# Kernel tuning notes

Measured on AMD Instinct MI355X. Metric: run time of the kernel, lower is better.

Reference implementation:

```python
import jax, jax.numpy as jnp
import numpy as np

K = 3
STRIDE = 1
PAD = 1
C_IN = 128
C_OUT = 128
B, H, W = 4, 128, 128


def conv2d(x, w, b, stride, pad):
    # x: (B,C,H,W), w: (O,I,kh,kw)
    out = jax.lax.conv_general_dilated(
        x, w, window_strides=(stride, stride),
        padding=[(pad, pad), (pad, pad)],
        dimension_numbers=("NCHW", "OIHW", "NCHW"))
    return out + b[None, :, None, None]


def bilinear_sample(img, ix, iy):
    # img: (C,H,W); ix, iy: (N,) float pixel coords.
    # Bilinear, padding_mode='zeros', align_corners=False semantics.
    C, Hc, Wc = img.shape
    x0 = jnp.floor(ix).astype(jnp.int32)
    y0 = jnp.floor(iy).astype(jnp.int32)
    x1 = x0 + 1
    y1 = y0 + 1
    wx1 = ix - x0.astype(img.dtype)
    wy1 = iy - y0.astype(img.dtype)
    wx0 = 1.0 - wx1
    wy0 = 1.0 - wy1

    def gather(yi, xi):
        valid = ((yi >= 0) & (yi < Hc) & (xi >= 0) & (xi < Wc)).astype(img.dtype)
        v = img[:, jnp.clip(yi, 0, Hc - 1), jnp.clip(xi, 0, Wc - 1)]  # (C,N)
        return v * valid[None, :]

    return (gather(y0, x0) * (wy0 * wx0)[None]
            + gather(y0, x1) * (wy0 * wx1)[None]
            + gather(y1, x0) * (wy1 * wx0)[None]
            + gather(y1, x1) * (wy1 * wx1)[None])


def setup_inputs() -> dict:
    key = jax.random.key(0)
    k1, k2, k3 = jax.random.split(key, 3)
    x = jax.random.normal(k1, (B, C_IN, H, W), dtype=jnp.float32)
    # offset conv: small random so grid_sample does real irregular gathers
    w_off = jax.random.normal(k2, (2 * K * K, C_IN, K, K), dtype=jnp.float32) * 0.01
    b_off = jnp.zeros((2 * K * K,), dtype=jnp.float32)
    # main conv: kaiming normal, fan_out = C_OUT*K*K
    std = float(np.sqrt(2.0 / (C_OUT * K * K)))
    w_main = jax.random.normal(k3, (C_OUT, C_IN, K, K), dtype=jnp.float32) * std
    b_main = jnp.zeros((C_OUT,), dtype=jnp.float32)
    return {"x": x, "w_off": w_off, "b_off": b_off,
            "w_main": w_main, "b_main": b_main}


def reference(x, w_off, b_off, w_main, b_main):
    Bx, C, Hx, Wx = x.shape
    off = conv2d(x, w_off, b_off, STRIDE, PAD)        # (B, 2*K*K, Ho, Wo)
    Ho, Wo = off.shape[2], off.shape[3]
    off = off.transpose(0, 2, 3, 1).reshape(Bx, Ho, Wo, K, K, 2)
    # snake cumulative offsets: x-offset cumsum over kernel row i, y over col j
    off_x = jnp.cumsum(off[..., 0], axis=3)           # over first kernel dim
    off_y = jnp.cumsum(off[..., 1], axis=4)           # over second kernel dim
    off = jnp.stack([off_x, off_y], axis=-1).reshape(Bx, Ho, Wo, K * K, 2)

    yr = jnp.linspace(-1.0, 1.0, Ho, dtype=x.dtype)
    xr = jnp.linspace(-1.0, 1.0, Wo, dtype=x.dtype)
    yg, xg = jnp.meshgrid(yr, xr, indexing="ij")
    base = jnp.stack([xg, yg], axis=-1)[None, :, :, None, :]  # (1,Ho,Wo,1,2)
    grid = (base + off).reshape(Bx, -1, 2)            # (B, Ho*Wo*K*K, 2)

    # unnormalize (align_corners=False)
    ix = ((grid[..., 0] + 1.0) * Wx - 1.0) * 0.5
    iy = ((grid[..., 1] + 1.0) * Hx - 1.0) * 0.5
    sampled = jax.vmap(bilinear_sample)(x, ix, iy)    # (B, C, Ho*Wo*K*K)
    sampled = sampled.reshape(Bx, C, Ho, Wo, K * K)

    w = w_main.reshape(w_main.shape[0], C, K * K)     # (O, C, K*K)
    out = jnp.einsum("bchwk,ock->bohw", sampled, w)
    return out + b_main[None, :, None, None]
```

## Files before the change

kernel.cpp:

```cpp
#include <hip/hip_runtime.h>
#include <cstddef>

#define Bb   4
#define CI   128
#define CO   128
#define Hh   128
#define Ww   128
#define HW   (Hh*Ww)
#define NOFF 18
#define NTAP 9
#define KTOT (NTAP*CI)
#define NSTEP 36

typedef short short8 __attribute__((ext_vector_type(8)));
typedef _Float16 half8 __attribute__((ext_vector_type(8)));
typedef float floatx4 __attribute__((ext_vector_type(4)));

__device__ inline unsigned short bf16_rne_bits(float f) {
    unsigned u = __float_as_uint(f);
    unsigned r = u + 0x7FFFu + ((u >> 16) & 1u);
    return (unsigned short)(r >> 16);
}
__device__ inline float bf16_bits_to_f32(unsigned short h) {
    return __uint_as_float((unsigned)h << 16);
}
__device__ inline unsigned short f32_to_f16_bits(float f) {
    union { _Float16 h; unsigned short u; } cv;
    cv.h = (_Float16)f;
    return cv.u;
}

__global__ __launch_bounds__(256) void k_transpose(const float* __restrict__ x,
                                                   _Float16* __restrict__ xt16,
                                                   unsigned short* __restrict__ xbh,
                                                   unsigned short* __restrict__ xbl) {
    __shared__ float tile[32][33];
    int b  = blockIdx.z;
    int c0 = blockIdx.y * 32;
    int p0 = blockIdx.x * 32;
    int tx = threadIdx.x;
    int ty = threadIdx.y;
    const float* xb = x + (size_t)b * CI * HW;
    size_t obase = (size_t)b * HW * CI;
#pragma unroll
    for (int i = 0; i < 4; ++i) {
        int c = c0 + ty + 8 * i;
        tile[ty + 8 * i][tx] = xb[(size_t)c * HW + p0 + tx];
    }
    __syncthreads();
#pragma unroll
    for (int i = 0; i < 4; ++i) {
        int p = p0 + ty + 8 * i;
        float v = tile[tx][ty + 8 * i];
        size_t o = obase + (size_t)p * CI + c0 + tx;
        xt16[o] = (_Float16)v;
        unsigned short hb = bf16_rne_bits(v);
        xbh[o] = hb;
        xbl[o] = bf16_rne_bits(v - bf16_bits_to_f32(hb));
    }
}

__global__ __launch_bounds__(256) void k_weights(const float* __restrict__ w_off,
                                                 const float* __restrict__ w_main,
                                                 unsigned short* __restrict__ wofh,
                                                 unsigned short* __restrict__ wofl,
                                                 unsigned short* __restrict__ wf16) {
    int idx = blockIdx.x * 256 + threadIdx.x;
    int stride = gridDim.x * 256;
    for (int i = idx; i < 9 * 4 * 2 * 512; i += stride) {
        int j  = i & 7;
        int l  = (i >> 3) & 63;
        int nt = (i >> 9) & 1;
        int ks = (i >> 10) & 3;
        int t  = i >> 12;
        int oc = nt * 16 + (l & 15);
        int c  = ks * 32 + (l >> 4) * 8 + j;
        float f = (oc < NOFF) ? w_off[(oc * CI + c) * 9 + t] : 0.f;
        unsigned short hb = bf16_rne_bits(f);
        wofh[i] = hb;
        wofl[i] = bf16_rne_bits(f - bf16_bits_to_f32(hb));
    }
    for (int i = idx; i < CO * KTOT; i += stride) {
        int j  = i & 7;
        int l  = (i >> 3) & 63;
        int g  = (i >> 9) & 7;
        int ks = (i >> 12) & 3;
        int t  = i >> 14;
        int o  = g * 16 + (l & 15);
        int c  = ks * 32 + (l >> 4) * 8 + j;
        wf16[i] = f32_to_f16_bits(w_main[(o * CI + c) * 9 + t]);
    }
}

__global__ __launch_bounds__(256, 2) void k_offsets(const unsigned short* __restrict__ xbh,
                                                    const unsigned short* __restrict__ xbl,
                                                    const unsigned short* __restrict__ wofh,
                                                    const unsigned short* __restrict__ wofl,
                                                    const float* __restrict__ b_off,
                                                    float2* __restrict__ coords) {
    __shared__ __align__(16) unsigned short ph[3 * 18 * 128];
    __shared__ __align__(16) unsigned short pl[3 * 18 * 128];
    __shared__ float rawp[2][16][19];
    int blk = blockIdx.x;
    int wt  = blk & 7;
    int h   = (blk >> 3) & 127;
    int b   = blk >> 10;
    int w0  = wt * 16;
    int tid  = threadIdx.x;
    int lane = tid & 63;
    int wave = tid >> 6;

    size_t xb0 = (size_t)b * HW * CI;
    for (int i = tid; i < 3 * 18 * 64; i += 256) {
        int c2  = i & 63;
        int col = (i >> 6) % 18;
        int r   = i / (18 * 64);
        int gy  = h - 1 + r;
        int gx  = w0 - 1 + col;
        unsigned vh = 0, vl = 0;
        if (gy >= 0 && gy < Hh && gx >= 0 && gx < Ww) {
            size_t o = xb0 + ((size_t)gy * Ww + gx) * CI + c2 * 2;
            vh = *(const unsigned*)(xbh + o);
            vl = *(const unsigned*)(xbl + o);
        }
        int byte = (((r * 18 + col) * 128) + c2 * 2) * 2;
        byte ^= (col & 7) << 4;
        *(unsigned*)((char*)ph + byte) = vh;
        *(unsigned*)((char*)pl + byte) = vl;
    }
    __syncthreads();

    int nt  = wave & 1;
    int th  = wave >> 1;
    int l15 = lane & 15, lhi = lane >> 4;
    floatx4 accE = (floatx4){0.f, 0.f, 0.f, 0.f};
    floatx4 accO = (floatx4){0.f, 0.f, 0.f, 0.f};
    const short8* bhp = (const short8*)wofh;
    const short8* blp = (const short8*)wofl;

#define TAP_STEP(t)                                                              \
    {                                                                            \
        const int ki = (t) / 3, kj = (t) % 3;                                    \
        int colb = l15 + kj;                                                     \
        int rowoff = (ki * 18 + colb) * 256;                                     \
        _Pragma("unroll")                                                        \
        for (int ks = 0; ks < 4; ++ks) {                                         \
            int abyte = (rowoff + ks * 64 + lhi * 16) ^ ((colb & 7) << 4);       \
            short8 Ah = *(const short8*)((char*)ph + abyte);                     \
            short8 Al = *(const short8*)((char*)pl + abyte);                     \
            size_t bi = (size_t)(((t) * 4 + ks) * 2 + nt) * 64 + lane;           \
            short8 Bh = bhp[bi];                                                 \
            short8 Bl = blp[bi];                                                 \
            floatx4& a = (ks & 1) ? accO : accE;                                 \
            a = __builtin_amdgcn_mfma_f32_16x16x32_bf16(Ah, Bh, a, 0, 0, 0);     \
            a = __builtin_amdgcn_mfma_f32_16x16x32_bf16(Ah, Bl, a, 0, 0, 0);     \
            a = __builtin_amdgcn_mfma_f32_16x16x32_bf16(Al, Bh, a, 0, 0, 0);     \
        }                                                                        \
    }
    if (th == 0) {
        TAP_STEP(0) TAP_STEP(1) TAP_STEP(2) TAP_STEP(3)
    } else {
        TAP_STEP(4) TAP_STEP(5) TAP_STEP(6) TAP_STEP(7) TAP_STEP(8)
    }
#undef TAP_STEP

    int oc = nt * 16 + l15;
    if (oc < NOFF) {
        float bo = (th == 0) ? b_off[oc] : 0.f;
#pragma unroll
        for (int r = 0; r < 4; ++r) {
            int px = lhi * 4 + r;
            rawp[th][px][oc] = (accE[r] + accO[r]) + bo;
        }
    }
    __syncthreads();

    for (int i = tid; i < 16 * NTAP; i += 256) {
        int px = i / NTAP;
        int t  = i % NTAP;
        int ki = t / 3, kj = t % 3;
        float offx = 0.f, offy = 0.f;
        for (int q = 0; q <= ki; ++q) {
            int idx = q * 6 + kj * 2 + 0;
            offx += rawp[0][px][idx] + rawp[1][px][idx];
        }
        for (int q = 0; q <= kj; ++q) {
            int idx = ki * 6 + q * 2 + 1;
            offy += rawp[0][px][idx] + rawp[1][px][idx];
        }
        int wg = w0 + px;
        float xg = -1.0f + 2.0f * (float)wg / 127.0f;
        float yg = -1.0f + 2.0f * (float)h  / 127.0f;
        float gxn = xg + offx;
        float gyn = yg + offy;
        float ix = ((gxn + 1.0f) * (float)Ww - 1.0f) * 0.5f;
        float iy = ((gyn + 1.0f) * (float)Hh - 1.0f) * 0.5f;
        coords[(((size_t)b * Hh + h) * Ww + wg) * NTAP + t] = make_float2(ix, iy);
    }
}

__global__ __launch_bounds__(256) void k_sample(const _Float16* __restrict__ xt16,
                                                const float2* __restrict__ coords,
                                                unsigned short* __restrict__ af16,
                                                int q0) {
    int nb = gridDim.x;
    int blkid = blockIdx.x;
    int cpx = nb >> 3;
    blkid = (blkid & 7) * cpx + (blkid >> 3);
    int task = blkid * 4 + (threadIdx.x >> 6);
    int lane = threadIdx.x & 63;
    int Pl   = task / 36;
    int rem  = task - Pl * 36;
    int tap  = rem >> 2;
    int ks   = rem & 3;
    int r = lane & 15, q = lane >> 4;
    int p = q0 + Pl * 16 + r;
    int b = p >> 14;

    float2 co = coords[(size_t)p * NTAP + tap];
    float ix = co.x, iy = co.y;
    float fx0 = floorf(ix), fy0 = floorf(iy);
    int x0 = (int)fx0, y0 = (int)fy0;
    int x1 = x0 + 1,   y1 = y0 + 1;
    float wx1 = ix - fx0, wy1 = iy - fy0;
    float wx0 = 1.f - wx1, wy0 = 1.f - wy1;
    bool vx0 = (x0 >= 0) & (x0 < Ww);
    bool vx1 = (x1 >= 0) & (x1 < Ww);
    bool vy0 = (y0 >= 0) & (y0 < Hh);
    bool vy1 = (y1 >= 0) & (y1 < Hh);
    int cx0 = min(max(x0, 0), Ww - 1), cx1 = min(max(x1, 0), Ww - 1);
    int cy0 = min(max(y0, 0), Hh - 1), cy1 = min(max(y1, 0), Hh - 1);
    float w00 = (vy0 && vx0) ? wy0 * wx0 : 0.f;
    float w01 = (vy0 && vx1) ? wy0 * wx1 : 0.f;
    float w10 = (vy1 && vx0) ? wy1 * wx0 : 0.f;
    float w11 = (vy1 && vx1) ? wy1 * wx1 : 0.f;

    const _Float16* xb  = xt16 + (size_t)b * HW * CI + ks * 32 + q * 8;
    half8 a8 = *(const half8*)(xb + ((size_t)cy0 * Ww + cx0) * CI);
    half8 b8 = *(const half8*)(xb + ((size_t)cy0 * Ww + cx1) * CI);
    half8 c8 = *(const half8*)(xb + ((size_t)cy1 * Ww + cx0) * CI);
    half8 d8 = *(const half8*)(xb + ((size_t)cy1 * Ww + cx1) * CI);
    short8 hv;
#pragma unroll
    for (int j = 0; j < 8; ++j) {
        float v = w00 * (float)a8[j] + w01 * (float)b8[j]
                + w10 * (float)c8[j] + w11 * (float)d8[j];
        hv[j] = (short)f32_to_f16_bits(v);
    }
    *(short8*)(af16 + ((size_t)task * 64 + lane) * 8) = hv;
}

__global__ __launch_bounds__(256, 4) void k_gemm(const unsigned short* __restrict__ af16,
                                                 const unsigned short* __restrict__ wf16,
                                                 const float* __restrict__ b_main,
                                                 float* __restrict__ out, int q0) {
    __shared__ __align__(16) float epi[CO * 33];
    int nb = gridDim.x;
    int cpx = nb >> 3;
    int blk = blockIdx.x;
    blk = (blk & 7) * cpx + (blk >> 3);
    int tid = threadIdx.x, lane = tid & 63, wave = tid >> 6;
    int wave_n = wave & 1, wave_m = wave >> 1;
    int l15 = lane & 15, lhi = lane >> 4;
    int P = blk * 2 + wave_m;

    const half8* ah = (const half8*)af16 + (size_t)P * NSTEP * 64 + lane;
    const half8* bh = (const half8*)wf16 + (size_t)wave_n * 4 * 64 + lane;

    floatx4 acc[4];
#pragma unroll
    for (int n = 0; n < 4; ++n) acc[n] = (floatx4){0.f, 0.f, 0.f, 0.f};

    half8 A0, B0[4], A1, B1[4];
    A0 = ah[0];
#pragma unroll
    for (int n = 0; n < 4; ++n) B0[n] = bh[(size_t)n * 64];

#pragma unroll 2
    for (int s = 0; s < NSTEP; s += 2) {
        A1 = ah[(size_t)(s + 1) * 64];
#pragma unroll
        for (int n = 0; n < 4; ++n) B1[n] = bh[(size_t)((s + 1) * 8 + n) * 64];
#pragma unroll
        for (int n = 0; n < 4; ++n)
            acc[n] = __builtin_amdgcn_mfma_f32_16x16x32_f16(A0, B0[n], acc[n], 0, 0, 0);
        if (s + 2 < NSTEP) {
            A0 = ah[(size_t)(s + 2) * 64];
#pragma unroll
            for (int n = 0; n < 4; ++n) B0[n] = bh[(size_t)((s + 2) * 8 + n) * 64];
        }
#pragma unroll
        for (int n = 0; n < 4; ++n)
            acc[n] = __builtin_amdgcn_mfma_f32_16x16x32_f16(A1, B1[n], acc[n], 0, 0, 0);
    }

#pragma unroll
    for (int n = 0; n < 4; ++n) {
        int o = wave_n * 64 + n * 16 + l15;
#pragma unroll
        for (int rr = 0; rr < 4; ++rr) {
            int px = wave_m * 16 + lhi * 4 + rr;
            epi[o * 33 + px] = acc[n][rr];
        }
    }
    __syncthreads();
    int p_blk = q0 + blk * 32;
    int b = p_blk >> 14, hw = p_blk & 16383;
    float* ob = out + (size_t)b * CO * HW + hw;
    for (int i = tid; i < CO * 32; i += 256) {
        int o  = i >> 5;
        int px = i & 31;
        __builtin_nontemporal_store(epi[o * 33 + px] + b_main[o],
                                    &ob[(size_t)o * HW + px]);
    }
}

extern "C" void kernel_launch(void* const* d_in, const int* in_sizes, int n_in,
                              void* d_out, int out_size, void* d_ws, size_t ws_size,
                              hipStream_t stream) {
    const float* x      = (const float*)d_in[0];
    const float* w_off  = (const float*)d_in[1];
    const float* b_off  = (const float*)d_in[2];
    const float* w_main = (const float*)d_in[3];
    const float* b_main = (const float*)d_in[4];
    float* out = (float*)d_out;

    char* base = (char*)d_ws;
    _Float16*       xt16 = (_Float16*)base;
    unsigned short* xbh  = (unsigned short*)(base + 16777216);
    unsigned short* xbl  = (unsigned short*)(base + 2 * 16777216);
    float2*         coords = (float2*)(base + 3 * 16777216);
    unsigned short* wofh = (unsigned short*)(base + 3 * 16777216 + 4718592);
    unsigned short* wofl = wofh + 9 * 4 * 2 * 512;
    unsigned short* wf16 = wofl + 9 * 4 * 2 * 512;
    size_t fixed_b = 3ull * 16777216 + 4718592
                   + 2 * (9 * 4 * 2 * 512) * 2 + (size_t)CO * KTOT * 2;
    unsigned short* af16 = (unsigned short*)(base + fixed_b);

    size_t avail = (ws_size > fixed_b) ? (ws_size - fixed_b) : 0;
    long long maxpx = (long long)(avail / 2304);
    int chunk = (int)((maxpx / 2048) * 2048);
    if (chunk > 32768) chunk = 32768;
    if (chunk < 2048) chunk = 2048;

    k_transpose<<<dim3(HW / 32, CI / 32, Bb), dim3(32, 8), 0, stream>>>(x, xt16, xbh, xbl);
    k_weights<<<576, 256, 0, stream>>>(w_off, w_main, wofh, wofl, wf16);
    k_offsets<<<Bb * Hh * (Ww / 16), 256, 0, stream>>>(xbh, xbl, wofh, wofl, b_off, coords);
    for (int q0 = 0; q0 < Bb * HW; q0 += chunk) {
        int np = Bb * HW - q0; if (np > chunk) np = chunk;
        k_sample<<<(np / 16) * 9, 256, 0, stream>>>(xt16, coords, af16, q0);
        k_gemm<<<np / 32, 256, 0, stream>>>(af16, wf16, b_main, out, q0);
    }
}
```

Before: 192.1 us.

## Software-pipeline offset, sample and GEMM stages via fused heterogeneous launches

Replaces the sequential offsets kernel and the per-chunk sample/GEMM loop with launches that mix block roles. Each launch runs one stage on one chunk (GEMM or offsets) alongside the next stage on the following chunk (sampling), using two ping-pong activation buffers. The goal is to fill the GPU with independent work and cut idle tails between dependent kernels. The chunk size is now fixed at 16384 and two buffers are used, so the code assumes a larger workspace. Launch bounds are also shared across roles, which may hurt occupancy for some of them.

```diff
diff --git a/kernel.cpp b/kernel.cpp
--- a/kernel.cpp
+++ b/kernel.cpp
@@ -11,6 +11,11 @@
 #define NTAP 9
 #define KTOT (NTAP*CI)
 #define NSTEP 36
+
+#define CHUNK 16384
+#define NSAMP ((CHUNK/16)*9)
+#define NGEMM (CHUNK/32)
+#define NOFFH ((Bb*HW/16)/2)
 
 typedef short short8 __attribute__((ext_vector_type(8)));
 typedef _Float16 half8 __attribute__((ext_vector_type(8)));
@@ -92,16 +97,16 @@
     }
 }
 
-__global__ __launch_bounds__(256, 2) void k_offsets(const unsigned short* __restrict__ xbh,
-                                                    const unsigned short* __restrict__ xbl,
-                                                    const unsigned short* __restrict__ wofh,
-                                                    const unsigned short* __restrict__ wofl,
-                                                    const float* __restrict__ b_off,
-                                                    float2* __restrict__ coords) {
+__device__ __forceinline__ void dev_offsets(int blk,
+                                            const unsigned short* __restrict__ xbh,
+                                            const unsigned short* __restrict__ xbl,
+                                            const unsigned short* __restrict__ wofh,
+                                            const unsigned short* __restrict__ wofl,
+                                            const float* __restrict__ b_off,
+                                            float2* __restrict__ coords) {
     __shared__ __align__(16) unsigned short ph[3 * 18 * 128];
     __shared__ __align__(16) unsigned short pl[3 * 18 * 128];
     __shared__ float rawp[2][16][19];
-    int blk = blockIdx.x;
     int wt  = blk & 7;
     int h   = (blk >> 3) & 127;
     int b   = blk >> 10;
@@ -199,14 +204,13 @@
     }
 }
 
-__global__ __launch_bounds__(256) void k_sample(const _Float16* __restrict__ xt16,
-                                                const float2* __restrict__ coords,
-                                                unsigned short* __restrict__ af16,
-                                                int q0) {
-    int nb = gridDim.x;
-    int blkid = blockIdx.x;
+__device__ __forceinline__ void dev_sample(int bid, int nb,
+                                           const _Float16* __restrict__ xt16,
+                                           const float2* __restrict__ coords,
+                                           unsigned short* __restrict__ af16,
+                                           int q0) {
     int cpx = nb >> 3;
-    blkid = (blkid & 7) * cpx + (blkid >> 3);
+    int blkid = (bid & 7) * cpx + (bid >> 3);
     int task = blkid * 4 + (threadIdx.x >> 6);
     int lane = threadIdx.x & 63;
     int Pl   = task / 36;
@@ -235,7 +239,7 @@
     float w10 = (vy1 && vx0) ? wy1 * wx0 : 0.f;
     float w11 = (vy1 && vx1) ? wy1 * wx1 : 0.f;
 
-    const _Float16* xb  = xt16 + (size_t)b * HW * CI + ks * 32 + q * 8;
+    const _Float16* xb = xt16 + (size_t)b * HW * CI + ks * 32 + q * 8;
     half8 a8 = *(const half8*)(xb + ((size_t)cy0 * Ww + cx0) * CI);
     half8 b8 = *(const half8*)(xb + ((size_t)cy0 * Ww + cx1) * CI);
     half8 c8 = *(const half8*)(xb + ((size_t)cy1 * Ww + cx0) * CI);
@@ -250,15 +254,14 @@
     *(short8*)(af16 + ((size_t)task * 64 + lane) * 8) = hv;
 }
 
-__global__ __launch_bounds__(256, 4) void k_gemm(const unsigned short* __restrict__ af16,
-                                                 const unsigned short* __restrict__ wf16,
-                                                 const float* __restrict__ b_main,
-                                                 float* __restrict__ out, int q0) {
+__device__ __forceinline__ void dev_gemm(int bid, int nb,
+                                         const unsigned short* __restrict__ af16,
+                                         const unsigned short* __restrict__ wf16,
+                                         const float* __restrict__ b_main,
+                                         float* __restrict__ out, int q0) {
     __shared__ __align__(16) float epi[CO * 33];
-    int nb = gridDim.x;
     int cpx = nb >> 3;
-    int blk = blockIdx.x;
-    blk = (blk & 7) * cpx + (blk >> 3);
+    int blk = (bid & 7) * cpx + (bid >> 3);
     int tid = threadIdx.x, lane = tid & 63, wave = tid >> 6;
     int wave_n = wave & 1, wave_m = wave >> 1;
     int l15 = lane & 15, lhi = lane >> 4;
@@ -313,6 +316,42 @@
         __builtin_nontemporal_store(epi[o * 33 + px] + b_main[o],
                                     &ob[(size_t)o * HW + px]);
     }
+}
+
+__global__ __launch_bounds__(256, 2) void k_offsets_part(
+        const unsigned short* xbh, const unsigned short* xbl,
+        const unsigned short* wofh, const unsigned short* wofl,
+        const float* b_off, float2* coords, int blk0) {
+    dev_offsets(blockIdx.x + blk0, xbh, xbl, wofh, wofl, b_off, coords);
+}
+
+__global__ __launch_bounds__(256, 2) void k_pair_os(
+        const _Float16* xt16, const float2* coords, unsigned short* af_s, int q0s,
+        const unsigned short* xbh, const unsigned short* xbl,
+        const unsigned short* wofh, const unsigned short* wofl,
+        const float* b_off, float2* coords_w, int off_blk0) {
+    if ((int)blockIdx.x < NSAMP)
+        dev_sample(blockIdx.x, NSAMP, xt16, coords, af_s, q0s);
+    else
+        dev_offsets((int)blockIdx.x - NSAMP + off_blk0, xbh, xbl, wofh, wofl,
+                    b_off, coords_w);
+}
+
+__global__ __launch_bounds__(256, 4) void k_pair_sg(
+        const unsigned short* af_g, int q0g,
+        unsigned short* af_s, int q0s,
+        const _Float16* xt16, const float2* coords,
+        const unsigned short* wf16, const float* b_main, float* out) {
+    if ((int)blockIdx.x < NGEMM)
+        dev_gemm(blockIdx.x, NGEMM, af_g, wf16, b_main, out, q0g);
+    else
+        dev_sample((int)blockIdx.x - NGEMM, NSAMP, xt16, coords, af_s, q0s);
+}
+
+__global__ __launch_bounds__(256, 4) void k_gemm_p(
+        const unsigned short* af_g, const unsigned short* wf16,
+        const float* b_main, float* out, int q0) {
+    dev_gemm(blockIdx.x, NGEMM, af_g, wf16, b_main, out, q0);
 }
 
 extern "C" void kernel_launch(void* const* d_in, const int* in_sizes, int n_in,
@@ -335,20 +374,21 @@
     unsigned short* wf16 = wofl + 9 * 4 * 2 * 512;
     size_t fixed_b = 3ull * 16777216 + 4718592
                    + 2 * (9 * 4 * 2 * 512) * 2 + (size_t)CO * KTOT * 2;
-    unsigned short* af16 = (unsigned short*)(base + fixed_b);
-
-    size_t avail = (ws_size > fixed_b) ? (ws_size - fixed_b) : 0;
-    long long maxpx = (long long)(avail / 2304);
-    int chunk = (int)((maxpx / 2048) * 2048);
-    if (chunk > 32768) chunk = 32768;
-    if (chunk < 2048) chunk = 2048;
+    unsigned short* afA = (unsigned short*)(base + fixed_b);
+    unsigned short* afB = afA + (size_t)CHUNK * KTOT;
 
     k_transpose<<<dim3(HW / 32, CI / 32, Bb), dim3(32, 8), 0, stream>>>(x, xt16, xbh, xbl);
     k_weights<<<576, 256, 0, stream>>>(w_off, w_main, wofh, wofl, wf16);
-    k_offsets<<<Bb * Hh * (Ww / 16), 256, 0, stream>>>(xbh, xbl, wofh, wofl, b_off, coords);
-    for (int q0 = 0; q0 < Bb * HW; q0 += chunk) {
-        int np = Bb * HW - q0; if (np > chunk) np = chunk;
-        k_sample<<<(np / 16) * 9, 256, 0, stream>>>(xt16, coords, af16, q0);
-        k_gemm<<<np / 32, 256, 0, stream>>>(af16, wf16, b_main, out, q0);
-    }
-}
+
+    k_offsets_part<<<NOFFH, 256, 0, stream>>>(xbh, xbl, wofh, wofl, b_off, coords, 0);
+    k_pair_os<<<NSAMP + NOFFH, 256, 0, stream>>>(xt16, coords, afA, 0,
+                                                 xbh, xbl, wofh, wofl, b_off,
+                                                 coords, NOFFH);
+    k_pair_sg<<<NGEMM + NSAMP, 256, 0, stream>>>(afA, 0,        afB, CHUNK,
+                                                 xt16, coords, wf16, b_main, out);
+    k_pair_sg<<<NGEMM + NSAMP, 256, 0, stream>>>(afB, CHUNK,    afA, 2 * CHUNK,
+                                                 xt16, coords, wf16, b_main, out);
+    k_pair_sg<<<NGEMM + NSAMP, 256, 0, stream>>>(afA, 2 * CHUNK, afB, 3 * CHUNK,
+                                                 xt16, coords, wf16, b_main, out);
+    k_gemm_p<<<NGEMM, 256, 0, stream>>>(afB, wf16, b_main, out, 3 * CHUNK);
+}
```

After: 193.6 us. No clear change (+0.8%).
